# Kernel optimization log

Hardware: AMD Instinct MI355X
Metric: run time of the kernel (lower is better)

## Reference

```python
import jax, jax.numpy as jnp
import numpy as np

V, D, NH, HD, FF, NL, NLOOPS = 1056, 320, 5, 64, 864, 6, 8
CAP, EPS, THETA = 0.8, 1e-6, 10000.0
B, S = 8, 2048


def rmsnorm(x, w):
    return w * (x * jax.lax.rsqrt(jnp.mean(x * x, axis=-1, keepdims=True) + EPS))


def rotate_half(x):
    x1, x2 = jnp.split(x, 2, axis=-1)
    return jnp.concatenate([-x2, x1], axis=-1)


def rope_tables(seq_len):
    freqs = 1.0 / (THETA ** (jnp.arange(0, HD, 2, dtype=jnp.float32) / HD))  # [HD/2]
    t = jnp.arange(seq_len, dtype=jnp.float32)
    f = jnp.outer(t, freqs)                      # [S, HD/2]
    f = jnp.concatenate([f, f], axis=-1)         # [S, HD]
    return jnp.cos(f), jnp.sin(f)


def setup_inputs() -> dict:
    key = jax.random.key(0)
    ks = jax.random.split(key, 12)
    std = 0.02
    inp = {
        "input_ids": jax.random.randint(ks[0], (B, S), 0, V),
        "iteration": 0,
        "embedding": jax.random.normal(ks[1], (V, D), jnp.float32),
        "iter_emb": jax.random.normal(ks[2], (NLOOPS, D), jnp.float32),
        "attn_norm_w": jnp.ones((NL, D), jnp.float32),
        "Wqkv": jax.random.normal(ks[3], (NL, 3 * D, D), jnp.float32) * std,
        "wo_w": jax.random.normal(ks[4], (NL, D, D), jnp.float32) * std,
        "router_w": jax.random.normal(ks[5], (NL, D), jnp.float32) * std,
        "mlp_norm_w": jnp.ones((NL, D), jnp.float32),
        "gate_w": jax.random.normal(ks[6], (NL, FF, D), jnp.float32) * std,
        "up_w": jax.random.normal(ks[7], (NL, FF, D), jnp.float32) * std,
        "down_w": jax.random.normal(ks[8], (NL, D, FF), jnp.float32) * std,
        "final_norm_w": jnp.ones((D,), jnp.float32),
    }
    return inp


def reference(input_ids, iteration, embedding, iter_emb, attn_norm_w, Wqkv, wo_w,
              router_w, mlp_norm_w, gate_w, up_w, down_w, final_norm_w):
    batch, seq = input_ids.shape
    k = max(1, int(seq * CAP))
    cos, sin = rope_tables(seq)                 # [S, HD]
    cos4 = cos[None, :, None, :]                # [1,S,1,HD]
    sin4 = sin[None, :, None, :]

    x = embedding[input_ids]                    # [B,S,D]
    if iteration < NLOOPS:
        x = x + iter_emb[iteration][None, None, :]

    causal = jnp.tril(jnp.ones((seq, seq), dtype=bool))
    bidx = jnp.arange(batch)[:, None]           # [B,1]

    for l in range(NL):
        # --- attention block ---
        h = rmsnorm(x, attn_norm_w[l])
        qkv = (h @ Wqkv[l].T).reshape(batch, seq, 3, NH, HD)
        q, kk, v = qkv[:, :, 0], qkv[:, :, 1], qkv[:, :, 2]   # [B,S,H,HD]
        q = q * cos4 + rotate_half(q) * sin4
        kk = kk * cos4 + rotate_half(kk) * sin4
        q, kk, v = (t.transpose(0, 2, 1, 3) for t in (q, kk, v))  # [B,H,S,HD]
        scores = jnp.einsum("bhqd,bhkd->bhqk", q, kk) / np.sqrt(HD)
        scores = jnp.where(causal, scores, -jnp.inf)
        attn = jax.nn.softmax(scores, axis=-1)
        out = jnp.einsum("bhqk,bhkd->bhqd", attn, v)
        out = out.transpose(0, 2, 1, 3).reshape(batch, seq, D)
        x = x + out @ wo_w[l].T

        # --- MoD router + SwiGLU MLP on selected tokens ---
        probs = jax.nn.sigmoid(x @ router_w[l])            # [B,S]
        topk_probs, topk_idx = jax.lax.top_k(probs, k)     # [B,K]
        sel = jnp.take_along_axis(x, topk_idx[:, :, None], axis=1)  # [B,K,D]
        hs = rmsnorm(sel, mlp_norm_w[l])
        gate = jax.nn.silu(hs @ gate_w[l].T) * (hs @ up_w[l].T)
        mlp = (gate @ down_w[l].T) * topk_probs[:, :, None]         # [B,K,D]
        x = x.at[bidx, topk_idx].add(mlp)                  # unique idx: add == scatter-set+residual

    return rmsnorm(x, final_norm_w)
```

## Files before the change

kernel.cpp:

```cpp
#include <hip/hip_runtime.h>
#include <hip/hip_bf16.h>
#include <math.h>

#define VSZ 1056
#define DD 320
#define NH 5
#define HD 64
#define FF 864
#define NL 6
#define NLOOPS 8
#define BB 8
#define SL 2048
#define KK 1638
#define EPSF 1e-6f

typedef _Float16 f16x8 __attribute__((ext_vector_type(8)));
typedef _Float16 f16x4 __attribute__((ext_vector_type(4)));
typedef float floatx16 __attribute__((ext_vector_type(16)));

__device__ inline void gll16(const void* g, void* l) {
    __builtin_amdgcn_global_load_lds((const __attribute__((address_space(1))) void*)g,
                                     (__attribute__((address_space(3))) void*)l, 16, 0, 0);
}

__global__ __launch_bounds__(256) void cast4_kernel(const float* __restrict__ s,
        _Float16* __restrict__ d, int n4) {
    int i = blockIdx.x * 256 + threadIdx.x;
    if (i >= n4) return;
    float4 v = ((const float4*)s)[i];
    f16x4 o = { (_Float16)v.x, (_Float16)v.y, (_Float16)v.z, (_Float16)v.w };
    *(f16x4*)(d + (size_t)i * 4) = o;
}

__global__ __launch_bounds__(256) void rope_init_kernel(float2* __restrict__ tab) {
    int i = blockIdx.x * 256 + threadIdx.x;
    int s = i >> 5, j = i & 31;
    float freq = exp2f(-(float)j * 0.4152410118609203f);
    float ang = (float)s * freq;
    tab[i] = make_float2(cosf(ang), sinf(ang));
}

__global__ __launch_bounds__(256) void embed_kernel(const int* __restrict__ ids,
        const int* __restrict__ iter, const float* __restrict__ emb,
        const float* __restrict__ iter_emb, float* __restrict__ x) {
    int i = blockIdx.x * 256 + threadIdx.x;
    int d = i % DD, bs = i / DD;
    float v = emb[(size_t)ids[bs] * DD + d];
    int it = iter[0];
    if (it < NLOOPS) v += iter_emb[it * DD + d];
    x[i] = v;
}

template<typename OT>
__global__ __launch_bounds__(256) void rmsnorm_kernel(const float* __restrict__ x,
        const float* __restrict__ w, OT* __restrict__ out, int nrows) {
    int row = blockIdx.x * 4 + (threadIdx.x >> 6);
    int lane = threadIdx.x & 63;
    if (row >= nrows) return;
    const float* xr = x + (size_t)row * DD;
    float v[5]; float ss = 0.f;
#pragma unroll
    for (int i = 0; i < 5; ++i) { v[i] = xr[lane + i * 64]; ss += v[i] * v[i]; }
#pragma unroll
    for (int o = 32; o > 0; o >>= 1) ss += __shfl_xor(ss, o);
    float r = rsqrtf(ss * (1.f / DD) + EPSF);
    OT* orow = out + (size_t)row * DD;
#pragma unroll
    for (int i = 0; i < 5; ++i) orow[lane + i * 64] = (OT)(w[lane + i * 64] * v[i] * r);
}

__global__ __launch_bounds__(256) void gather_rmsnorm_kernel(const float* __restrict__ x,
        const int* __restrict__ tkidx, const float* __restrict__ w,
        _Float16* __restrict__ out, int nrows) {
    int row = blockIdx.x * 4 + (threadIdx.x >> 6);
    int lane = threadIdx.x & 63;
    if (row >= nrows) return;
    int b = row / KK;
    int t = tkidx[row];
    const float* xr = x + ((size_t)b * SL + t) * DD;
    float v[5]; float ss = 0.f;
#pragma unroll
    for (int i = 0; i < 5; ++i) { v[i] = xr[lane + i * 64]; ss += v[i] * v[i]; }
#pragma unroll
    for (int o = 32; o > 0; o >>= 1) ss += __shfl_xor(ss, o);
    float r = rsqrtf(ss * (1.f / DD) + EPSF);
    _Float16* orow = out + (size_t)row * DD;
#pragma unroll
    for (int i = 0; i < 5; ++i) orow[lane + i * 64] = (_Float16)(w[lane + i * 64] * v[i] * r);
}

__global__ __launch_bounds__(256) void router_kernel(const float* __restrict__ x,
        const float* __restrict__ rw, float* __restrict__ probs, int nrows) {
    int row = blockIdx.x * 4 + (threadIdx.x >> 6);
    int lane = threadIdx.x & 63;
    if (row >= nrows) return;
    const float* xr = x + (size_t)row * DD;
    float ss = 0.f;
#pragma unroll
    for (int i = 0; i < 5; ++i) ss += xr[lane + i * 64] * rw[lane + i * 64];
#pragma unroll
    for (int o = 32; o > 0; o >>= 1) ss += __shfl_xor(ss, o);
    if (lane == 0) probs[row] = 1.f / (1.f + __expf(-ss));
}

__global__ __launch_bounds__(1024) void topk_kernel(const float* __restrict__ probs,
        int* __restrict__ tkidx, float* __restrict__ tkprob) {
    __shared__ int hist[256];
    __shared__ int scn[256];
    __shared__ int outc;
    __shared__ int s_digit, s_rem;
    int b = blockIdx.x, tid = threadIdx.x;
    unsigned long long k0, k1;
    {
        unsigned int f0 = __float_as_uint(probs[b * SL + tid]);
        unsigned int f1 = __float_as_uint(probs[b * SL + tid + 1024]);
        k0 = ((unsigned long long)f0 << 32) | (unsigned int)(2047 - tid);
        k1 = ((unsigned long long)f1 << 32) | (unsigned int)(2047 - (tid + 1024));
    }
    if (tid == 0) outc = 0;
    unsigned long long prefix = 0, pmask = 0;
    int target = KK;
    for (int shift = 56; shift >= 0; shift -= 8) {
        if (tid < 256) hist[tid] = 0;
        __syncthreads();
        bool a0 = (k0 & pmask) == prefix;
        bool a1 = (k1 & pmask) == prefix;
        int d0 = (int)((k0 >> shift) & 255);
        int d1 = (int)((k1 >> shift) & 255);
        if (a0) atomicAdd(&hist[d0], 1);
        if (a1) atomicAdd(&hist[d1], 1);
        __syncthreads();
        if (tid < 64) {
            int h0 = hist[tid * 4], h1 = hist[tid * 4 + 1];
            int h2 = hist[tid * 4 + 2], h3 = hist[tid * 4 + 3];
            int s3 = h3, s2 = h2 + s3, s1 = h1 + s2, s0 = h0 + s1;
            int s = s0;
#pragma unroll
            for (int off = 1; off < 64; off <<= 1) {
                int v = __shfl_down(s, off);
                if (tid + off >= 64) v = 0;
                s += v;
            }
            int A = s - s0;
            scn[tid * 4]     = s0 + A;
            scn[tid * 4 + 1] = s1 + A;
            scn[tid * 4 + 2] = s2 + A;
            scn[tid * 4 + 3] = s3 + A;
        }
        __syncthreads();
        if (tid < 256 && hist[tid] > 0) {
            int S = scn[tid];
            int Sgt = S - hist[tid];
            if (Sgt < target && target <= S) { s_digit = tid; s_rem = target - Sgt; }
        }
        __syncthreads();
        int dsel = s_digit, rem = s_rem;
        bool full = (rem == hist[dsel]);
        if (a0 && (d0 > dsel || (full && d0 == dsel))) {
            int s = atomicAdd(&outc, 1);
            tkidx[b * KK + s] = 2047 - (int)(k0 & 0xffffffffu);
            tkprob[b * KK + s] = __uint_as_float((unsigned int)(k0 >> 32));
        }
        if (a1 && (d1 > dsel || (full && d1 == dsel))) {
            int s = atomicAdd(&outc, 1);
            tkidx[b * KK + s] = 2047 - (int)(k1 & 0xffffffffu);
            tkprob[b * KK + s] = __uint_as_float((unsigned int)(k1 >> 32));
        }
        if (full) break;
        target = rem;
        prefix |= ((unsigned long long)dsel) << shift;
        pmask  |= ((unsigned long long)255) << shift;
        __syncthreads();
    }
}

__global__ __launch_bounds__(256) void prep_kernel(const _Float16* __restrict__ qkv,
        const float2* __restrict__ ropet,
        _Float16* __restrict__ Qh, _Float16* __restrict__ Kt, _Float16* __restrict__ Vt) {
    __shared__ _Float16 vt[64][72];
    int tid = threadIdx.x;
    int t = blockIdx.x, h = blockIdx.y, b = blockIdx.z;
    int bh = b * NH + h;
    int c = tid >> 5;
    int slb = tid & 31;
    const float QS = 0.125f * 1.44269504088896341f;
#pragma unroll
    for (int half = 0; half < 2; ++half) {
        int sl = half * 32 + slb;
        int s = t * 64 + sl;
        size_t rbase = ((size_t)(b * SL + s) * 3) * (NH * 64) + h * 64;
        f16x8 qv = *(const f16x8*)(qkv + rbase + c * 8);
        f16x8 qp = *(const f16x8*)(qkv + rbase + (c ^ 4) * 8);
        f16x8 kv = *(const f16x8*)(qkv + rbase + NH * 64 + c * 8);
        f16x8 kp = *(const f16x8*)(qkv + rbase + NH * 64 + (c ^ 4) * 8);
        f16x8 vv = *(const f16x8*)(qkv + rbase + 2 * NH * 64 + c * 8);
        const float2* rp = ropet + (size_t)s * 32 + (c & 3) * 8;
        f16x8 qo, ko;
#pragma unroll
        for (int j = 0; j < 8; ++j) {
            int d = c * 8 + j;
            float2 cs = rp[j];
            float cc = cs.x, sn = cs.y;
            float a = (float)qv[j], p = (float)qp[j];
            float ka = (float)kv[j], kb2 = (float)kp[j];
            float qr = (d < 32) ? a * cc - p * sn : a * cc + p * sn;
            float kr = (d < 32) ? ka * cc - kb2 * sn : ka * cc + kb2 * sn;
            qo[j] = (_Float16)(qr * QS);
            ko[j] = (_Float16)kr;
        }
        *(f16x8*)(Qh + ((size_t)bh * SL + s) * 64 + c * 8) = qo;
        *(f16x8*)(Kt + (((size_t)bh * 32 + t) * 8 + c) * 512 + sl * 8) = ko;
        *(f16x8*)(&vt[sl][c * 8]) = vv;
    }
    __syncthreads();
#pragma unroll
    for (int gg = 0; gg < 2; ++gg) {
        int oo = tid * 16 + gg * 8;
        int kc = oo >> 9;
        int d = (oo >> 3) & 63;
        f16x8 vo;
#pragma unroll
        for (int j = 0; j < 8; ++j) {
            int key = (kc >> 1) * 16 + (j & 3) + 8 * (j >> 2) + 4 * (kc & 1);
            vo[j] = vt[key][d];
        }
        *(f16x8*)(Vt + (((size_t)bh * 32 + t) * 8 + kc) * 512 + d * 8) = vo;
    }
}

__global__ __launch_bounds__(256, 2) void attn_mfma(const _Float16* __restrict__ Qh,
        const _Float16* __restrict__ Kt, const _Float16* __restrict__ Vt,
        _Float16* __restrict__ attn_out) {
    __shared__ float red[4][32][32];
    __shared__ float msh[4][32];
    __shared__ float lsh[4][32];
    int tid = threadIdx.x;
    int w = tid >> 6;
    int lane = tid & 63;
    int l31 = lane & 31, h5 = lane >> 5;
    int g = blockIdx.x;
    int j = g >> 3;
    int bh = (g & 7) + 8 * (j >> 6);
    int qt = 63 - (j & 63);
    int b = bh / NH, h = bh % NH;
    int nt = (qt >> 1) + 1;
    int qw = qt * 32;
    int myq = qw + l31;

    f16x8 qf[4];
    const _Float16* qrow = Qh + ((size_t)bh * SL + myq) * 64;
#pragma unroll
    for (int kd = 0; kd < 4; ++kd) qf[kd] = *(const f16x8*)(qrow + kd * 16 + h5 * 8);

    const _Float16* Kb = Kt + (size_t)bh * 32 * 4096;
    const _Float16* Vb = Vt + (size_t)bh * 32 * 4096;

    floatx16 O0, O1;
#pragma unroll
    for (int r = 0; r < 16; ++r) { O0[r] = 0.f; O1[r] = 0.f; }
    float m = -INFINITY, l = 0.f;

    for (int t = w; t < nt; t += 4) {
        const _Float16* kb = Kb + (size_t)t * 4096;
        const _Float16* vb = Vb + (size_t)t * 4096;
        f16x8 a0[4], a1[4], v0[4], v1[4];
#pragma unroll
        for (int kd = 0; kd < 4; ++kd) {
            int off = (kd * 2 + h5) * 512 + l31 * 8;
            a0[kd] = *(const f16x8*)(kb + off);
            a1[kd] = *(const f16x8*)(kb + off + 256);
        }
#pragma unroll
        for (int kc = 0; kc < 4; ++kc) {
            int off = (kc * 2 + h5) * 512 + l31 * 8;
            v0[kc] = *(const f16x8*)(vb + off);
            v1[kc] = *(const f16x8*)(vb + off + 256);
        }
        floatx16 S0, S1;
#pragma unroll
        for (int r = 0; r < 16; ++r) { S0[r] = 0.f; S1[r] = 0.f; }
#pragma unroll
        for (int kd = 0; kd < 4; ++kd) {
            S0 = __builtin_amdgcn_mfma_f32_32x32x16_f16(a0[kd], qf[kd], S0, 0, 0, 0);
            S1 = __builtin_amdgcn_mfma_f32_32x32x16_f16(a1[kd], qf[kd], S1, 0, 0, 0);
        }
        int t0 = t * 64;
        if (t0 + 63 > qw) {
#pragma unroll
            for (int r = 0; r < 16; ++r) {
                int key = t0 + (r & 3) + 8 * (r >> 2) + 4 * h5;
                if (key > myq) S0[r] = -INFINITY;
                if (key + 32 > myq) S1[r] = -INFINITY;
            }
        }
        float tmax = S0[0];
#pragma unroll
        for (int r = 1; r < 16; ++r) tmax = fmaxf(tmax, S0[r]);
#pragma unroll
        for (int r = 0; r < 16; ++r) tmax = fmaxf(tmax, S1[r]);
        tmax = fmaxf(tmax, __shfl_xor(tmax, 32));
        if (__any(tmax > m + 8.f)) {
            float mnew = fmaxf(m, tmax);
            float alpha = exp2f(m - mnew);
            l *= alpha; O0 *= alpha; O1 *= alpha; m = mnew;
        }
        float P0[16], P1[16]; float psum = 0.f;
#pragma unroll
        for (int r = 0; r < 16; ++r) { P0[r] = exp2f(S0[r] - m); psum += P0[r]; }
#pragma unroll
        for (int r = 0; r < 16; ++r) { P1[r] = exp2f(S1[r] - m); psum += P1[r]; }
        psum += __shfl_xor(psum, 32);
        l += psum;
#pragma unroll
        for (int sub = 0; sub < 2; ++sub) {
            const float* P = sub ? P1 : P0;
#pragma unroll
            for (int kc = 0; kc < 2; ++kc) {
                auto q01 = __builtin_amdgcn_cvt_pkrtz(P[kc * 8 + 0], P[kc * 8 + 1]);
                auto q23 = __builtin_amdgcn_cvt_pkrtz(P[kc * 8 + 2], P[kc * 8 + 3]);
                auto q45 = __builtin_amdgcn_cvt_pkrtz(P[kc * 8 + 4], P[kc * 8 + 5]);
                auto q67 = __builtin_amdgcn_cvt_pkrtz(P[kc * 8 + 6], P[kc * 8 + 7]);
                f16x8 pf;
                pf[0] = (_Float16)q01[0]; pf[1] = (_Float16)q01[1];
                pf[2] = (_Float16)q23[0]; pf[3] = (_Float16)q23[1];
                pf[4] = (_Float16)q45[0]; pf[5] = (_Float16)q45[1];
                pf[6] = (_Float16)q67[0]; pf[7] = (_Float16)q67[1];
                int ksg = sub * 2 + kc;
                O0 = __builtin_amdgcn_mfma_f32_32x32x16_f16(v0[ksg], pf, O0, 0, 0, 0);
                O1 = __builtin_amdgcn_mfma_f32_32x32x16_f16(v1[ksg], pf, O1, 0, 0, 0);
            }
        }
    }
    if (h5 == 0) msh[w][l31] = m;
    __syncthreads();
    float M = fmaxf(fmaxf(msh[0][l31], msh[1][l31]), fmaxf(msh[2][l31], msh[3][l31]));
    float wgt = exp2f(m - M);
    if (h5 == 0) lsh[w][l31] = l * wgt;
#pragma unroll
    for (int r = 0; r < 16; ++r) {
        int d = (r & 3) + 8 * (r >> 2) + 4 * h5;
        red[w][d][l31] = O0[r] * wgt;
    }
    __syncthreads();
    float lsum = lsh[0][l31] + lsh[1][l31] + lsh[2][l31] + lsh[3][l31];
    float linv = 1.f / lsum;
    if (w < 2) {
        f16x8 ov;
#pragma unroll
        for (int k = 0; k < 8; ++k) {
            int d = w * 16 + h5 * 8 + k;
            ov[k] = (_Float16)((red[0][d][l31] + red[1][d][l31] +
                                red[2][d][l31] + red[3][d][l31]) * linv);
        }
        *(f16x8*)(attn_out + ((size_t)(b * SL + myq)) * DD + h * 64 + w * 16 + h5 * 8) = ov;
    }
    __syncthreads();
#pragma unroll
    for (int r = 0; r < 16; ++r) {
        int d = (r & 3) + 8 * (r >> 2) + 4 * h5;
        red[w][d][l31] = O1[r] * wgt;
    }
    __syncthreads();
    if (w >= 2) {
        f16x8 ov;
#pragma unroll
        for (int k = 0; k < 8; ++k) {
            int d = (w - 2) * 16 + h5 * 8 + k;
            ov[k] = (_Float16)((red[0][d][l31] + red[1][d][l31] +
                                red[2][d][l31] + red[3][d][l31]) * linv);
        }
        *(f16x8*)(attn_out + ((size_t)(b * SL + myq)) * DD + h * 64 + 32 + (w - 2) * 16 + h5 * 8) = ov;
    }
}

__global__ __launch_bounds__(256) void gemm_qkv(const _Float16* __restrict__ A,
        const _Float16* __restrict__ W, _Float16* __restrict__ Ch,
        int M, int N, int K, int nn_tiles) {
    __shared__ __attribute__((aligned(16))) _Float16 As[2][2048];
    __shared__ __attribute__((aligned(16))) _Float16 Ws[2][4096];
    int tid = threadIdx.x;
    int lane = tid & 63;
    int wave = tid >> 6;
    int l31 = lane & 31, h5 = lane >> 5;
    int nwg = gridDim.x;
    int q = nwg >> 3, r = nwg & 7;
    int xcd = blockIdx.x & 7, idx = blockIdx.x >> 3;
    int wgid = (xcd < r ? xcd * (q + 1) : r * (q + 1) + (xcd - r) * q) + idx;
    int mt = wgid / nn_tiles;
    int nt = wgid - mt * nn_tiles;
    int m0 = mt * 64, n0 = nt * 128;
    int wm = (wave & 1) * 32, wn2 = (wave >> 1) * 64;

    int srA = tid & 63, skA = tid >> 6;
    int srW = tid & 127, skW = tid >> 7;
    int arow = m0 + srA; if (arow >= M) arow = M - 1;
    int wrow = n0 + srW; if (wrow >= N) wrow = N - 1;
    const _Float16* Ag = A + (size_t)arow * K + skA * 8;
    const _Float16* Wg = W + (size_t)wrow * K + skW * 8;
    _Float16* AsD = As[0] + (size_t)(tid & ~63) * 8;
    _Float16* WsD = Ws[0] + (size_t)(tid & ~63) * 8;

    floatx16 acc0, acc1;
#pragma unroll
    for (int i = 0; i < 16; ++i) { acc0[i] = 0.f; acc1[i] = 0.f; }

    gll16(Ag, AsD);
    gll16(Wg, WsD);
    gll16(Wg + 16, WsD + 2048);
    __syncthreads();

    int nk = K >> 5;
    for (int t = 0; t < nk; ++t) {
        int buf = t & 1;
        if (t + 1 < nk) {
            int k0 = (t + 1) * 32;
            int bo = buf ^ 1;
            gll16(Ag + k0, AsD + bo * 2048);
            gll16(Wg + k0, WsD + bo * 4096);
            gll16(Wg + k0 + 16, WsD + bo * 4096 + 2048);
        }
        const _Float16* Asb = As[buf];
        const _Float16* Wsb = Ws[buf];
#pragma unroll
        for (int ks = 0; ks < 2; ++ks) {
            int kc = ks * 2 + h5;
            f16x8 a  = *(const f16x8*)(Asb + kc * 512 + (wm + l31) * 8);
            f16x8 b0 = *(const f16x8*)(Wsb + kc * 1024 + (wn2 + l31) * 8);
            f16x8 b1 = *(const f16x8*)(Wsb + kc * 1024 + (wn2 + 32 + l31) * 8);
            acc0 = __builtin_amdgcn_mfma_f32_32x32x16_f16(a, b0, acc0, 0, 0, 0);
            acc1 = __builtin_amdgcn_mfma_f32_32x32x16_f16(a, b1, acc1, 0, 0, 0);
        }
        __syncthreads();
    }

#pragma unroll
    for (int nj = 0; nj < 2; ++nj) {
        int nn = n0 + wn2 + nj * 32 + l31;
        if (nn >= N) continue;
        const floatx16& ac = nj ? acc1 : acc0;
#pragma unroll
        for (int r2 = 0; r2 < 16; ++r2) {
            int mm = m0 + wm + (r2 & 3) + 8 * (r2 >> 2) + 4 * h5;
            if (mm >= M) continue;
            Ch[(size_t)mm * N + nn] = (_Float16)ac[r2];
        }
    }
}

template<int MODE>
__global__ __launch_bounds__(256) void gemm_mfma(const _Float16* __restrict__ A,
        const _Float16* __restrict__ W, _Float16* __restrict__ Ch, float* __restrict__ X,
        int M, int N, int K, int nn_tiles, const int* __restrict__ sidx, const float* __restrict__ sprob) {
    __shared__ __attribute__((aligned(16))) _Float16 As[2][4096];
    __shared__ __attribute__((aligned(16))) _Float16 Ws[2][4096];
    int tid = threadIdx.x;
    int lane = tid & 63;
    int wave = tid >> 6;
    int l31 = lane & 31, h5 = lane >> 5;
    int nwg = gridDim.x;
    int q = nwg >> 3, r = nwg & 7;
    int xcd = blockIdx.x & 7, idx = blockIdx.x >> 3;
    int wgid = (xcd < r ? xcd * (q + 1) : r * (q + 1) + (xcd - r) * q) + idx;
    int mt = wgid / nn_tiles;
    int nt = wgid - mt * nn_tiles;
    int m0 = mt * 64, n0 = nt * 64;
    int wm = (wave & 1) * 32, wn = (wave >> 1) * 32;

    int srow = tid & 63;
    int skc = tid >> 6;
    int arow = m0 + srow; if (arow >= M) arow = M - 1;
    int wrow = n0 + srow; if (wrow >= N) wrow = N - 1;
    const _Float16* Ag = A + (size_t)arow * K + skc * 8;
    const _Float16* Wg = W + (size_t)wrow * K + skc * 8;
    _Float16* AsD = As[0] + (size_t)(tid & ~63) * 8;
    _Float16* WsD = Ws[0] + (size_t)(tid & ~63) * 8;

    floatx16 acc;
#pragma unroll
    for (int i = 0; i < 16; ++i) acc[i] = 0.f;

    int nk32 = K >> 5;
    int nfull = nk32 >> 1;
    int tail = nk32 & 1;

    gll16(Ag, AsD);
    gll16(Wg, WsD);
    gll16(Ag + 32, AsD + 2048);
    gll16(Wg + 32, WsD + 2048);
    __syncthreads();

    for (int t = 0; t < nfull; ++t) {
        int buf = t & 1;
        int bo = (buf ^ 1) * 4096;
        if (t + 1 < nfull) {
            int k0 = (t + 1) * 64;
            gll16(Ag + k0, AsD + bo);
            gll16(Wg + k0, WsD + bo);
            gll16(Ag + k0 + 32, AsD + bo + 2048);
            gll16(Wg + k0 + 32, WsD + bo + 2048);
        } else if (tail) {
            int k0 = nfull * 64;
            gll16(Ag + k0, AsD + bo);
            gll16(Wg + k0, WsD + bo);
        }
        const _Float16* Asb = As[buf];
        const _Float16* Wsb = Ws[buf];
#pragma unroll
        for (int ks = 0; ks < 4; ++ks) {
            int kc = ks * 2 + h5;
            f16x8 a = *(const f16x8*)(Asb + kc * 512 + (wm + l31) * 8);
            f16x8 b = *(const f16x8*)(Wsb + kc * 512 + (wn + l31) * 8);
            acc = __builtin_amdgcn_mfma_f32_32x32x16_f16(a, b, acc, 0, 0, 0);
        }
        __syncthreads();
    }
    if (tail) {
        int buf = nfull & 1;
        const _Float16* Asb = As[buf];
        const _Float16* Wsb = Ws[buf];
#pragma unroll
        for (int ks = 0; ks < 2; ++ks) {
            int kc = ks * 2 + h5;
            f16x8 a = *(const f16x8*)(Asb + kc * 512 + (wm + l31) * 8);
            f16x8 b = *(const f16x8*)(Wsb + kc * 512 + (wn + l31) * 8);
            acc = __builtin_amdgcn_mfma_f32_32x32x16_f16(a, b, acc, 0, 0, 0);
        }
    }

    int nn = n0 + wn + l31;
#pragma unroll
    for (int r2 = 0; r2 < 16; ++r2) {
        int mm = m0 + wm + (r2 & 3) + 8 * (r2 >> 2) + 4 * h5;
        if (mm >= M || nn >= N) continue;
        float v = acc[r2];
        if (MODE == 1) {
            X[(size_t)mm * N + nn] += v;
        } else {
            int b = mm / KK;
            X[((size_t)(b * SL + sidx[mm])) * N + nn] += v * sprob[mm];
        }
    }
}

__global__ __launch_bounds__(256) void gemm_gateup(const _Float16* __restrict__ A,
        const _Float16* __restrict__ Wg, const _Float16* __restrict__ Wu,
        _Float16* __restrict__ Ch, int M, int N, int K, int nn_tiles) {
    __shared__ __attribute__((aligned(16))) _Float16 As[2][2048];
    __shared__ __attribute__((aligned(16))) _Float16 Wgs[2][4096];
    __shared__ __attribute__((aligned(16))) _Float16 Wus[2][4096];
    int tid = threadIdx.x;
    int lane = tid & 63;
    int wave = tid >> 6;
    int l31 = lane & 31, h5 = lane >> 5;
    int nwg = gridDim.x;
    int q = nwg >> 3, r = nwg & 7;
    int xcd = blockIdx.x & 7, idx = blockIdx.x >> 3;
    int wgid = (xcd < r ? xcd * (q + 1) : r * (q + 1) + (xcd - r) * q) + idx;
    int mt = wgid / nn_tiles;
    int nt = wgid - mt * nn_tiles;
    int m0 = mt * 64, n0 = nt * 128;
    int wm = (wave & 1) * 32, wn2 = (wave >> 1) * 64;

    int srA = tid & 63, skA = tid >> 6;
    int srW = tid & 127, skW = tid >> 7;
    int arow = m0 + srA; if (arow >= M) arow = M - 1;
    int wrow = n0 + srW; if (wrow >= N) wrow = N - 1;
    const _Float16* Ag  = A  + (size_t)arow * K + skA * 8;
    const _Float16* Wgg = Wg + (size_t)wrow * K + skW * 8;
    const _Float16* Wug = Wu + (size_t)wrow * K + skW * 8;
    _Float16* AsD  = As[0]  + (size_t)(tid & ~63) * 8;
    _Float16* WgsD = Wgs[0] + (size_t)(tid & ~63) * 8;
    _Float16* WusD = Wus[0] + (size_t)(tid & ~63) * 8;

    floatx16 ag0, ag1, au0, au1;
#pragma unroll
    for (int i = 0; i < 16; ++i) { ag0[i] = 0.f; ag1[i] = 0.f; au0[i] = 0.f; au1[i] = 0.f; }

    gll16(Ag, AsD);
    gll16(Wgg, WgsD);
    gll16(Wgg + 16, WgsD + 2048);
    gll16(Wug, WusD);
    gll16(Wug + 16, WusD + 2048);
    __syncthreads();

    int nk = K >> 5;
    for (int t = 0; t < nk; ++t) {
        int buf = t & 1;
        if (t + 1 < nk) {
            int k0 = (t + 1) * 32;
            int bo = buf ^ 1;
            gll16(Ag + k0, AsD + bo * 2048);
            gll16(Wgg + k0, WgsD + bo * 4096);
            gll16(Wgg + k0 + 16, WgsD + bo * 4096 + 2048);
            gll16(Wug + k0, WusD + bo * 4096);
            gll16(Wug + k0 + 16, WusD + bo * 4096 + 2048);
        }
        const _Float16* Asb = As[buf];
        const _Float16* Wgb = Wgs[buf];
        const _Float16* Wub = Wus[buf];
#pragma unroll
        for (int ks = 0; ks < 2; ++ks) {
            int kc = ks * 2 + h5;
            f16x8 a  = *(const f16x8*)(Asb + kc * 512 + (wm + l31) * 8);
            f16x8 g0 = *(const f16x8*)(Wgb + kc * 1024 + (wn2 + l31) * 8);
            f16x8 g1 = *(const f16x8*)(Wgb + kc * 1024 + (wn2 + 32 + l31) * 8);
            f16x8 u0 = *(const f16x8*)(Wub + kc * 1024 + (wn2 + l31) * 8);
            f16x8 u1 = *(const f16x8*)(Wub + kc * 1024 + (wn2 + 32 + l31) * 8);
            ag0 = __builtin_amdgcn_mfma_f32_32x32x16_f16(a, g0, ag0, 0, 0, 0);
            au0 = __builtin_amdgcn_mfma_f32_32x32x16_f16(a, u0, au0, 0, 0, 0);
            ag1 = __builtin_amdgcn_mfma_f32_32x32x16_f16(a, g1, ag1, 0, 0, 0);
            au1 = __builtin_amdgcn_mfma_f32_32x32x16_f16(a, u1, au1, 0, 0, 0);
        }
        __syncthreads();
    }

#pragma unroll
    for (int nj = 0; nj < 2; ++nj) {
        int nn = n0 + wn2 + nj * 32 + l31;
        if (nn >= N) continue;
        const floatx16& gA = nj ? ag1 : ag0;
        const floatx16& uA = nj ? au1 : au0;
#pragma unroll
        for (int r2 = 0; r2 < 16; ++r2) {
            int mm = m0 + wm + (r2 & 3) + 8 * (r2 >> 2) + 4 * h5;
            if (mm >= M) continue;
            float gv = gA[r2], uv = uA[r2];
            Ch[(size_t)mm * N + nn] = (_Float16)((gv / (1.f + __expf(-gv))) * uv);
        }
    }
}

extern "C" void kernel_launch(void* const* d_in, const int* in_sizes, int n_in,
                              void* d_out, int out_size, void* d_ws, size_t ws_size,
                              hipStream_t stream) {
    const int*   ids          = (const int*)d_in[0];
    const int*   iter         = (const int*)d_in[1];
    const float* emb          = (const float*)d_in[2];
    const float* iter_emb     = (const float*)d_in[3];
    const float* attn_norm_w  = (const float*)d_in[4];
    const float* Wqkv         = (const float*)d_in[5];
    const float* wo_w         = (const float*)d_in[6];
    const float* router_w     = (const float*)d_in[7];
    const float* mlp_norm_w   = (const float*)d_in[8];
    const float* gate_w       = (const float*)d_in[9];
    const float* up_w         = (const float*)d_in[10];
    const float* down_w       = (const float*)d_in[11];
    const float* final_norm_w = (const float*)d_in[12];
    float* out = (float*)d_out;

    const size_t XN   = (size_t)BB * SL * DD;
    const size_t QKVN = (size_t)BB * SL * 3 * DD;
    const size_t HN   = (size_t)BB * NH * SL * 64;
    char* ws = (char*)d_ws;
    size_t off = 0;
    float*    x        = (float*)(ws + off);    off += XN * 4;
    _Float16* h        = (_Float16*)(ws + off); off += XN * 2;
    _Float16* attn_out = (_Float16*)(ws + off); off += XN * 2;
    float*    probs    = (float*)(ws + off);    off += (size_t)BB * SL * 4;
    int*      tkidx    = (int*)(ws + off);      off += (size_t)BB * KK * 4;
    float*    tkprob   = (float*)(ws + off);    off += (size_t)BB * KK * 4;
    off = (off + 255) & ~(size_t)255;
    _Float16* qkvh     = (_Float16*)(ws + off); off += QKVN * 2;
    _Float16* Qh       = (_Float16*)(ws + off); off += HN * 2;
    _Float16* Kh       = (_Float16*)(ws + off); off += HN * 2;
    _Float16* Vh       = (_Float16*)(ws + off); off += HN * 2;
    float2*   ropet    = (float2*)(ws + off);   off += (size_t)SL * 32 * 8;
    _Float16* WqkvH    = (_Float16*)(ws + off);
    _Float16* woH   = WqkvH + (size_t)NL * 3 * DD * DD;
    _Float16* gateH = woH   + (size_t)NL * DD * DD;
    _Float16* upH   = gateH + (size_t)NL * FF * DD;
    _Float16* downH = upH   + (size_t)NL * FF * DD;
    _Float16* g1 = qkvh;

    rope_init_kernel<<<SL * 32 / 256, 256, 0, stream>>>(ropet);
    cast4_kernel<<<(NL * 3 * DD * DD / 4 + 255) / 256, 256, 0, stream>>>(Wqkv, WqkvH, NL * 3 * DD * DD / 4);
    cast4_kernel<<<(NL * DD * DD / 4 + 255) / 256, 256, 0, stream>>>(wo_w, woH, NL * DD * DD / 4);
    cast4_kernel<<<(NL * FF * DD / 4 + 255) / 256, 256, 0, stream>>>(gate_w, gateH, NL * FF * DD / 4);
    cast4_kernel<<<(NL * FF * DD / 4 + 255) / 256, 256, 0, stream>>>(up_w, upH, NL * FF * DD / 4);
    cast4_kernel<<<(NL * DD * FF / 4 + 255) / 256, 256, 0, stream>>>(down_w, downH, NL * DD * FF / 4);

    embed_kernel<<<20480, 256, 0, stream>>>(ids, iter, emb, iter_emb, x);

    const int M1 = BB * SL;
    const int M2 = BB * KK;
    const int MT1 = (M1 + 63) / 64;
    const int MT2 = (M2 + 63) / 64;
    for (int l = 0; l < NL; ++l) {
        rmsnorm_kernel<_Float16><<<4096, 256, 0, stream>>>(x, attn_norm_w + l * DD, h, M1);
        gemm_qkv<<<MT1 * 8, 256, 0, stream>>>(h, WqkvH + (size_t)l * 3 * DD * DD,
                                              qkvh, M1, 3 * DD, DD, 8);
        prep_kernel<<<dim3(SL / 64, NH, BB), 256, 0, stream>>>(qkvh, ropet, Qh, Kh, Vh);
        attn_mfma<<<BB * NH * (SL / 32), 256, 0, stream>>>(Qh, Kh, Vh, attn_out);
        gemm_mfma<1><<<MT1 * 5, 256, 0, stream>>>(attn_out, woH + (size_t)l * DD * DD,
                                                  nullptr, x, M1, DD, DD, 5, nullptr, nullptr);
        router_kernel<<<4096, 256, 0, stream>>>(x, router_w + l * DD, probs, M1);
        topk_kernel<<<BB, 1024, 0, stream>>>(probs, tkidx, tkprob);
        gather_rmsnorm_kernel<<<3276, 256, 0, stream>>>(x, tkidx, mlp_norm_w + l * DD, h, M2);
        gemm_gateup<<<MT2 * 7, 256, 0, stream>>>(h, gateH + (size_t)l * FF * DD,
                                                 upH + (size_t)l * FF * DD, g1, M2, FF, DD, 7);
        gemm_mfma<2><<<MT2 * 5, 256, 0, stream>>>(g1, downH + (size_t)l * DD * FF,
                                                  nullptr, x, M2, DD, FF, 5, tkidx, tkprob);
    }
    rmsnorm_kernel<float><<<4096, 256, 0, stream>>>(x, final_norm_w, out, M1);
}
```

Before: 1.538 ms.

## Give each wave its own query tile in attention, drop cross-wave LDS reduction

The attention kernel used to split one 32-query tile's key tiles across four waves and then merge their softmax states and outputs through shared memory with several barriers. Now each wave walks all key tiles for its own query tile, so the shared-memory reduction, barriers and max/sum rescaling disappear. The grid shrinks to a quarter of the blocks, and the occupancy hint is dropped from launch bounds. The running-max reduction is also rewritten as a shallower tree. In exchange there are fewer concurrent waves to hide latency, each wave has a longer serial loop, and the output is written with scattered 2-byte stores instead of 16-byte vector stores.

```diff
diff --git a/kernel.cpp b/kernel.cpp
--- a/kernel.cpp
+++ b/kernel.cpp
@@ -228,20 +228,18 @@
     }
 }
 
-__global__ __launch_bounds__(256, 2) void attn_mfma(const _Float16* __restrict__ Qh,
+__global__ __launch_bounds__(256) void attn_mfma(const _Float16* __restrict__ Qh,
         const _Float16* __restrict__ Kt, const _Float16* __restrict__ Vt,
         _Float16* __restrict__ attn_out) {
-    __shared__ float red[4][32][32];
-    __shared__ float msh[4][32];
-    __shared__ float lsh[4][32];
     int tid = threadIdx.x;
     int w = tid >> 6;
     int lane = tid & 63;
     int l31 = lane & 31, h5 = lane >> 5;
     int g = blockIdx.x;
     int j = g >> 3;
-    int bh = (g & 7) + 8 * (j >> 6);
-    int qt = 63 - (j & 63);
+    int job = j * 4 + w;
+    int bh = (g & 7) + 8 * (job >> 6);
+    int qt = 63 - (job & 63);
     int b = bh / NH, h = bh % NH;
     int nt = (qt >> 1) + 1;
     int qw = qt * 32;
@@ -260,7 +258,7 @@
     for (int r = 0; r < 16; ++r) { O0[r] = 0.f; O1[r] = 0.f; }
     float m = -INFINITY, l = 0.f;
 
-    for (int t = w; t < nt; t += 4) {
+    for (int t = 0; t < nt; ++t) {
         const _Float16* kb = Kb + (size_t)t * 4096;
         const _Float16* vb = Vb + (size_t)t * 4096;
         f16x8 a0[4], a1[4], v0[4], v1[4];
@@ -293,11 +291,22 @@
                 if (key + 32 > myq) S1[r] = -INFINITY;
             }
         }
-        float tmax = S0[0];
-#pragma unroll
-        for (int r = 1; r < 16; ++r) tmax = fmaxf(tmax, S0[r]);
-#pragma unroll
-        for (int r = 0; r < 16; ++r) tmax = fmaxf(tmax, S1[r]);
+        float r0 = fmaxf(fmaxf(S0[0], S0[1]), S0[2]);
+        float r1 = fmaxf(fmaxf(S0[3], S0[4]), S0[5]);
+        float r2 = fmaxf(fmaxf(S0[6], S0[7]), S0[8]);
+        float r3 = fmaxf(fmaxf(S0[9], S0[10]), S0[11]);
+        float r4 = fmaxf(fmaxf(S0[12], S0[13]), S0[14]);
+        float r5 = fmaxf(fmaxf(S0[15], S1[0]), S1[1]);
+        float r6 = fmaxf(fmaxf(S1[2], S1[3]), S1[4]);
+        float r7 = fmaxf(fmaxf(S1[5], S1[6]), S1[7]);
+        float r8 = fmaxf(fmaxf(S1[8], S1[9]), S1[10]);
+        float r9 = fmaxf(fmaxf(S1[11], S1[12]), S1[13]);
+        float ra = fmaxf(S1[14], S1[15]);
+        float s0 = fmaxf(fmaxf(r0, r1), r2);
+        float s1 = fmaxf(fmaxf(r3, r4), r5);
+        float s2 = fmaxf(fmaxf(r6, r7), r8);
+        float s3 = fmaxf(r9, ra);
+        float tmax = fmaxf(fmaxf(fmaxf(s0, s1), s2), s3);
         tmax = fmaxf(tmax, __shfl_xor(tmax, 32));
         if (__any(tmax > m + 8.f)) {
             float mnew = fmaxf(m, tmax);
@@ -331,45 +340,13 @@
             }
         }
     }
-    if (h5 == 0) msh[w][l31] = m;
-    __syncthreads();
-    float M = fmaxf(fmaxf(msh[0][l31], msh[1][l31]), fmaxf(msh[2][l31], msh[3][l31]));
-    float wgt = exp2f(m - M);
-    if (h5 == 0) lsh[w][l31] = l * wgt;
+    float linv = 1.f / l;
+    _Float16* orow = attn_out + ((size_t)(b * SL + myq)) * DD + h * 64;
 #pragma unroll
     for (int r = 0; r < 16; ++r) {
-        int d = (r & 3) + 8 * (r >> 2) + 4 * h5;
-        red[w][d][l31] = O0[r] * wgt;
-    }
-    __syncthreads();
-    float lsum = lsh[0][l31] + lsh[1][l31] + lsh[2][l31] + lsh[3][l31];
-    float linv = 1.f / lsum;
-    if (w < 2) {
-        f16x8 ov;
-#pragma unroll
-        for (int k = 0; k < 8; ++k) {
-            int d = w * 16 + h5 * 8 + k;
-            ov[k] = (_Float16)((red[0][d][l31] + red[1][d][l31] +
-                                red[2][d][l31] + red[3][d][l31]) * linv);
-        }
-        *(f16x8*)(attn_out + ((size_t)(b * SL + myq)) * DD + h * 64 + w * 16 + h5 * 8) = ov;
-    }
-    __syncthreads();
-#pragma unroll
-    for (int r = 0; r < 16; ++r) {
-        int d = (r & 3) + 8 * (r >> 2) + 4 * h5;
-        red[w][d][l31] = O1[r] * wgt;
-    }
-    __syncthreads();
-    if (w >= 2) {
-        f16x8 ov;
-#pragma unroll
-        for (int k = 0; k < 8; ++k) {
-            int d = (w - 2) * 16 + h5 * 8 + k;
-            ov[k] = (_Float16)((red[0][d][l31] + red[1][d][l31] +
-                                red[2][d][l31] + red[3][d][l31]) * linv);
-        }
-        *(f16x8*)(attn_out + ((size_t)(b * SL + myq)) * DD + h * 64 + 32 + (w - 2) * 16 + h5 * 8) = ov;
+        int dl = (r & 3) + 8 * (r >> 2) + 4 * h5;
+        orow[dl] = (_Float16)(O0[r] * linv);
+        orow[dl + 32] = (_Float16)(O1[r] * linv);
     }
 }
 
@@ -690,7 +667,7 @@
         gemm_qkv<<<MT1 * 8, 256, 0, stream>>>(h, WqkvH + (size_t)l * 3 * DD * DD,
                                               qkvh, M1, 3 * DD, DD, 8);
         prep_kernel<<<dim3(SL / 64, NH, BB), 256, 0, stream>>>(qkvh, ropet, Qh, Kh, Vh);
-        attn_mfma<<<BB * NH * (SL / 32), 256, 0, stream>>>(Qh, Kh, Vh, attn_out);
+        attn_mfma<<<BB * NH * (SL / 64) / 2, 256, 0, stream>>>(Qh, Kh, Vh, attn_out);
         gemm_mfma<1><<<MT1 * 5, 256, 0, stream>>>(attn_out, woH + (size_t)l * DD * DD,
                                                   nullptr, x, M1, DD, DD, 5, nullptr, nullptr);
         router_kernel<<<4096, 256, 0, stream>>>(x, router_w + l * DD, probs, M1);
```

New measurement: 1.724 ms. 12.1% more time.

## Fuse RoPE and QKV head-layout scatter into QKV GEMM epilogue

Applied to the files above, without the earlier changes.

Removes the separate prep kernel. The QKV GEMM epilogue now applies RoPE to Q and K, scales Q, and writes Q, K and V straight into the tiled attention layouts instead of staging a qkv buffer. It also merges the five weight-cast launches into one kernel. This avoids writing and re-reading the qkv intermediate and cuts launch count, but the epilogue stores become scattered 2-byte writes that may coalesce poorly. It also relies on each wave's 64-column slice lining up exactly with one head.

```diff
diff --git a/kernel.cpp b/kernel.cpp
--- a/kernel.cpp
+++ b/kernel.cpp
@@ -23,13 +23,24 @@
                                      (__attribute__((address_space(3))) void*)l, 16, 0, 0);
 }
 
-__global__ __launch_bounds__(256) void cast4_kernel(const float* __restrict__ s,
-        _Float16* __restrict__ d, int n4) {
+__global__ __launch_bounds__(256) void cast5_kernel(
+        const float* __restrict__ s1, const float* __restrict__ s2,
+        const float* __restrict__ s3, const float* __restrict__ s4,
+        const float* __restrict__ s5,
+        _Float16* __restrict__ d1, _Float16* __restrict__ d2,
+        _Float16* __restrict__ d3, _Float16* __restrict__ d4,
+        _Float16* __restrict__ d5,
+        int n1, int n2, int n3, int n4, int n5) {
     int i = blockIdx.x * 256 + threadIdx.x;
-    if (i >= n4) return;
-    float4 v = ((const float4*)s)[i];
+    const float* s; _Float16* d; int l = i;
+    if (l < n1) { s = s1; d = d1; }
+    else { l -= n1; if (l < n2) { s = s2; d = d2; }
+    else { l -= n2; if (l < n3) { s = s3; d = d3; }
+    else { l -= n3; if (l < n4) { s = s4; d = d4; }
+    else { l -= n4; if (l >= n5) return; s = s5; d = d5; } } } }
+    float4 v = ((const float4*)s)[l];
     f16x4 o = { (_Float16)v.x, (_Float16)v.y, (_Float16)v.z, (_Float16)v.w };
-    *(f16x4*)(d + (size_t)i * 4) = o;
+    *(f16x4*)(d + (size_t)l * 4) = o;
 }
 
 __global__ __launch_bounds__(256) void rope_init_kernel(float2* __restrict__ tab) {
@@ -171,60 +182,6 @@
         prefix |= ((unsigned long long)dsel) << shift;
         pmask  |= ((unsigned long long)255) << shift;
         __syncthreads();
-    }
-}
-
-__global__ __launch_bounds__(256) void prep_kernel(const _Float16* __restrict__ qkv,
-        const float2* __restrict__ ropet,
-        _Float16* __restrict__ Qh, _Float16* __restrict__ Kt, _Float16* __restrict__ Vt) {
-    __shared__ _Float16 vt[64][72];
-    int tid = threadIdx.x;
-    int t = blockIdx.x, h = blockIdx.y, b = blockIdx.z;
-    int bh = b * NH + h;
-    int c = tid >> 5;
-    int slb = tid & 31;
-    const float QS = 0.125f * 1.44269504088896341f;
-#pragma unroll
-    for (int half = 0; half < 2; ++half) {
-        int sl = half * 32 + slb;
-        int s = t * 64 + sl;
-        size_t rbase = ((size_t)(b * SL + s) * 3) * (NH * 64) + h * 64;
-        f16x8 qv = *(const f16x8*)(qkv + rbase + c * 8);
-        f16x8 qp = *(const f16x8*)(qkv + rbase + (c ^ 4) * 8);
-        f16x8 kv = *(const f16x8*)(qkv + rbase + NH * 64 + c * 8);
-        f16x8 kp = *(const f16x8*)(qkv + rbase + NH * 64 + (c ^ 4) * 8);
-        f16x8 vv = *(const f16x8*)(qkv + rbase + 2 * NH * 64 + c * 8);
-        const float2* rp = ropet + (size_t)s * 32 + (c & 3) * 8;
-        f16x8 qo, ko;
-#pragma unroll
-        for (int j = 0; j < 8; ++j) {
-            int d = c * 8 + j;
-            float2 cs = rp[j];
-            float cc = cs.x, sn = cs.y;
-            float a = (float)qv[j], p = (float)qp[j];
-            float ka = (float)kv[j], kb2 = (float)kp[j];
-            float qr = (d < 32) ? a * cc - p * sn : a * cc + p * sn;
-            float kr = (d < 32) ? ka * cc - kb2 * sn : ka * cc + kb2 * sn;
-            qo[j] = (_Float16)(qr * QS);
-            ko[j] = (_Float16)kr;
-        }
-        *(f16x8*)(Qh + ((size_t)bh * SL + s) * 64 + c * 8) = qo;
-        *(f16x8*)(Kt + (((size_t)bh * 32 + t) * 8 + c) * 512 + sl * 8) = ko;
-        *(f16x8*)(&vt[sl][c * 8]) = vv;
-    }
-    __syncthreads();
-#pragma unroll
-    for (int gg = 0; gg < 2; ++gg) {
-        int oo = tid * 16 + gg * 8;
-        int kc = oo >> 9;
-        int d = (oo >> 3) & 63;
-        f16x8 vo;
-#pragma unroll
-        for (int j = 0; j < 8; ++j) {
-            int key = (kc >> 1) * 16 + (j & 3) + 8 * (j >> 2) + 4 * (kc & 1);
-            vo[j] = vt[key][d];
-        }
-        *(f16x8*)(Vt + (((size_t)bh * 32 + t) * 8 + kc) * 512 + d * 8) = vo;
     }
 }
 
@@ -374,7 +331,8 @@
 }
 
 __global__ __launch_bounds__(256) void gemm_qkv(const _Float16* __restrict__ A,
-        const _Float16* __restrict__ W, _Float16* __restrict__ Ch,
+        const _Float16* __restrict__ W, const float2* __restrict__ ropet,
+        _Float16* __restrict__ Qh, _Float16* __restrict__ Kt, _Float16* __restrict__ Vt,
         int M, int N, int K, int nn_tiles) {
     __shared__ __attribute__((aligned(16))) _Float16 As[2][2048];
     __shared__ __attribute__((aligned(16))) _Float16 Ws[2][4096];
@@ -433,16 +391,41 @@
         __syncthreads();
     }
 
-#pragma unroll
-    for (int nj = 0; nj < 2; ++nj) {
-        int nn = n0 + wn2 + nj * 32 + l31;
-        if (nn >= N) continue;
-        const floatx16& ac = nj ? acc1 : acc0;
+    int nb0 = n0 + wn2;
+    if (nb0 >= N) return;
+    int comp = nb0 / DD;
+    int hh = (nb0 % DD) / 64;
+    const float QS = 0.125f * 1.44269504088896341f;
+    if (comp == 2) {
 #pragma unroll
         for (int r2 = 0; r2 < 16; ++r2) {
             int mm = m0 + wm + (r2 & 3) + 8 * (r2 >> 2) + 4 * h5;
-            if (mm >= M) continue;
-            Ch[(size_t)mm * N + nn] = (_Float16)ac[r2];
+            int b = mm >> 11, s = mm & 2047;
+            int key = s & 63;
+            int kc8 = ((key >> 4) << 1) | ((key >> 2) & 1);
+            int jj = (key & 3) | (((key >> 3) & 1) << 2);
+            size_t vbase = (((size_t)(b * NH + hh) * 32 + (s >> 6)) * 8 + kc8) * 512 + jj;
+            Vt[vbase + (size_t)l31 * 8] = (_Float16)acc0[r2];
+            Vt[vbase + (size_t)(l31 + 32) * 8] = (_Float16)acc1[r2];
+        }
+    } else {
+#pragma unroll
+        for (int r2 = 0; r2 < 16; ++r2) {
+            int mm = m0 + wm + (r2 & 3) + 8 * (r2 >> 2) + 4 * h5;
+            int b = mm >> 11, s = mm & 2047;
+            float2 cs = ropet[(size_t)s * 32 + l31];
+            float lo = acc0[r2], hi = acc1[r2];
+            float ro0 = lo * cs.x - hi * cs.y;
+            float ro1 = hi * cs.x + lo * cs.y;
+            if (comp == 0) {
+                _Float16* qp = Qh + ((size_t)(b * NH + hh) * SL + s) * 64;
+                qp[l31] = (_Float16)(ro0 * QS);
+                qp[l31 + 32] = (_Float16)(ro1 * QS);
+            } else {
+                size_t kb2 = (((size_t)(b * NH + hh) * 32 + (s >> 6)) * 8) * 512 + (s & 63) * 8;
+                Kt[kb2 + (size_t)(l31 >> 3) * 512 + (l31 & 7)] = (_Float16)ro0;
+                Kt[kb2 + (size_t)((l31 + 32) >> 3) * 512 + (l31 & 7)] = (_Float16)ro1;
+            }
         }
     }
 }
@@ -673,11 +656,14 @@
     _Float16* g1 = qkvh;
 
     rope_init_kernel<<<SL * 32 / 256, 256, 0, stream>>>(ropet);
-    cast4_kernel<<<(NL * 3 * DD * DD / 4 + 255) / 256, 256, 0, stream>>>(Wqkv, WqkvH, NL * 3 * DD * DD / 4);
-    cast4_kernel<<<(NL * DD * DD / 4 + 255) / 256, 256, 0, stream>>>(wo_w, woH, NL * DD * DD / 4);
-    cast4_kernel<<<(NL * FF * DD / 4 + 255) / 256, 256, 0, stream>>>(gate_w, gateH, NL * FF * DD / 4);
-    cast4_kernel<<<(NL * FF * DD / 4 + 255) / 256, 256, 0, stream>>>(up_w, upH, NL * FF * DD / 4);
-    cast4_kernel<<<(NL * DD * FF / 4 + 255) / 256, 256, 0, stream>>>(down_w, downH, NL * DD * FF / 4);
+    {
+        int n1 = NL * 3 * DD * DD / 4, n2 = NL * DD * DD / 4;
+        int n3 = NL * FF * DD / 4, n4 = NL * FF * DD / 4, n5 = NL * DD * FF / 4;
+        int ntot = n1 + n2 + n3 + n4 + n5;
+        cast5_kernel<<<(ntot + 255) / 256, 256, 0, stream>>>(
+            Wqkv, wo_w, gate_w, up_w, down_w,
+            WqkvH, woH, gateH, upH, downH, n1, n2, n3, n4, n5);
+    }
 
     embed_kernel<<<20480, 256, 0, stream>>>(ids, iter, emb, iter_emb, x);
 
@@ -688,8 +674,7 @@
     for (int l = 0; l < NL; ++l) {
         rmsnorm_kernel<_Float16><<<4096, 256, 0, stream>>>(x, attn_norm_w + l * DD, h, M1);
         gemm_qkv<<<MT1 * 8, 256, 0, stream>>>(h, WqkvH + (size_t)l * 3 * DD * DD,
-                                              qkvh, M1, 3 * DD, DD, 8);
-        prep_kernel<<<dim3(SL / 64, NH, BB), 256, 0, stream>>>(qkvh, ropet, Qh, Kh, Vh);
+                                              ropet, Qh, Kh, Vh, M1, 3 * DD, DD, 8);
         attn_mfma<<<BB * NH * (SL / 32), 256, 0, stream>>>(Qh, Kh, Vh, attn_out);
         gemm_mfma<1><<<MT1 * 5, 256, 0, stream>>>(attn_out, woH + (size_t)l * DD * DD,
                                                   nullptr, x, M1, DD, DD, 5, nullptr, nullptr);
```

New measurement: 1.484 ms, median of 2. -3.6%, faster.
